# Kernel optimization log

Measured on AMD Instinct MI355X. Metric: run time of the kernel, lower is better.

The kernel has to match this reference:

```python
import jax, jax.numpy as jnp
import numpy as np

N_Q = 32      # questions per batch
N_DOCS = 8    # docs per question (positive first)
Q_LEN = 32    # query tokens
D_LEN = 200   # doc tokens
DIM = 128     # ColBERT embedding dim


def setup_inputs() -> dict:
    key = jax.random.key(0)
    k1, k2 = jax.random.split(key)
    hq = jax.random.normal(k1, (N_Q, Q_LEN, DIM), dtype=jnp.float32)
    hd = jax.random.normal(k2, (N_Q * N_DOCS, D_LEN, DIM), dtype=jnp.float32)
    return {"hq": hq, "hd": hd}


def reference(hq, hd):
    # ColBERT maxsim: [n, m, q, d] token-level scores
    scores = jnp.einsum("nqh,mdh->nmqd", hq, hd)
    # max over doc tokens, mean over query tokens -> [n, m]
    score_matrix = jnp.max(scores, axis=-1).mean(axis=-1)

    n, m = score_matrix.shape
    n_docs = m // n
    # positive doc is the first in each group: targets = [0, n_docs, 2*n_docs, ...]
    targets = jnp.arange(0, m, n_docs)
    logp = jax.nn.log_softmax(score_matrix, axis=-1)
    loss = -jnp.mean(jnp.take_along_axis(logp, targets[:, None], axis=1))
    return score_matrix, loss
```

## Files before the change

kernel.cpp:

```cpp
#include <hip/hip_runtime.h>
#include <hip/hip_bf16.h>
#include <math.h>

typedef short short8 __attribute__((ext_vector_type(8)));
typedef float f32x4 __attribute__((ext_vector_type(4)));

#define NQ 32
#define NDOCS 8
#define QLEN 32
#define DLEN 200
#define DIM 128
#define MD 256
#define ROWB 256

__device__ __forceinline__ short f2bf(float x) {
    union { float f; unsigned u; } v; v.f = x;
    unsigned r = v.u + 0x7FFFu + ((v.u >> 16) & 1u);
    return (short)(r >> 16);
}

__device__ __forceinline__ short8 cvt8(float4 f0, float4 f1) {
    short8 o;
    o[0] = f2bf(f0.x); o[1] = f2bf(f0.y); o[2] = f2bf(f0.z); o[3] = f2bf(f0.w);
    o[4] = f2bf(f1.x); o[5] = f2bf(f1.y); o[6] = f2bf(f1.z); o[7] = f2bf(f1.w);
    return o;
}

__device__ __forceinline__ void writeChunk(char* lds, int c, float4 f0, float4 f1) {
    int row = c >> 4, kc = c & 15;
    int byte = row * ROWB + ((kc * 16) ^ ((row & 7) << 4));
    *reinterpret_cast<short8*>(&lds[byte]) = cvt8(f0, f1);
}

__global__ __launch_bounds__(1024, 4) void colbert_scores(const float* __restrict__ hd,
                                                          const float* __restrict__ hq,
                                                          float* __restrict__ out) {
    __shared__ char lds[208 * ROWB];
    const int m = blockIdx.x;
    const int tid = threadIdx.x;
    const float4* src4 = reinterpret_cast<const float4*>(hd + (size_t)m * (DLEN * DIM));

    for (int c = tid; c < 3200; c += 1024) {
        float4 f0 = src4[c * 2], f1 = src4[c * 2 + 1];
        writeChunk(lds, c, f0, f1);
    }
    if (tid < 128) {
        float4 z = {0.f, 0.f, 0.f, 0.f};
        writeChunk(lds, 3200 + tid, z, z);
    }

    const int wid = tid >> 6, lane = tid & 63;
    const int lg = lane >> 4, lr = lane & 15;
    const int n0 = wid * 2;
    const float4* hq4 = reinterpret_cast<const float4*>(hq);
    short8 a[2][2][4];
    #pragma unroll
    for (int nn = 0; nn < 2; ++nn)
        #pragma unroll
        for (int qt = 0; qt < 2; ++qt)
            #pragma unroll
            for (int s = 0; s < 4; ++s) {
                int e4 = ((n0 + nn) * QLEN + qt * 16 + lr) * (DIM / 4) + s * 8 + lg * 2;
                a[nn][qt][s] = cvt8(hq4[e4], hq4[e4 + 1]);
            }

    __syncthreads();

    int va[4];
    const int pre = ((lg ^ (lr & 7)) << 4);
    #pragma unroll
    for (int s = 0; s < 4; ++s) va[s] = lr * ROWB + (pre ^ (s << 6));

    float qmax00 = -INFINITY, qmax01 = -INFINITY, qmax10 = -INFINITY, qmax11 = -INFINITY;

#define STEP(DT, MASKED)                                                          \
    {                                                                             \
        f32x4 acc00 = {0,0,0,0}, acc01 = {0,0,0,0}, acc10 = {0,0,0,0}, acc11 = {0,0,0,0}; \
        _Pragma("unroll")                                                         \
        for (int s = 0; s < 4; ++s) {                                             \
            short8 b = *reinterpret_cast<const short8*>(&lds[va[s] + (DT) * 4096]); \
            acc00 = __builtin_amdgcn_mfma_f32_16x16x32_bf16(b, a[0][0][s], acc00, 0, 0, 0); \
            acc01 = __builtin_amdgcn_mfma_f32_16x16x32_bf16(b, a[0][1][s], acc01, 0, 0, 0); \
            acc10 = __builtin_amdgcn_mfma_f32_16x16x32_bf16(b, a[1][0][s], acc10, 0, 0, 0); \
            acc11 = __builtin_amdgcn_mfma_f32_16x16x32_bf16(b, a[1][1][s], acc11, 0, 0, 0); \
        }                                                                         \
        if (!(MASKED) || lg < 2) {                                                \
            qmax00 = fmaxf(qmax00, fmaxf(fmaxf(acc00[0], acc00[1]), fmaxf(acc00[2], acc00[3]))); \
            qmax01 = fmaxf(qmax01, fmaxf(fmaxf(acc01[0], acc01[1]), fmaxf(acc01[2], acc01[3]))); \
            qmax10 = fmaxf(qmax10, fmaxf(fmaxf(acc10[0], acc10[1]), fmaxf(acc10[2], acc10[3]))); \
            qmax11 = fmaxf(qmax11, fmaxf(fmaxf(acc11[0], acc11[1]), fmaxf(acc11[2], acc11[3]))); \
        }                                                                         \
    }

    #pragma unroll
    for (int dt = 0; dt < 12; ++dt) STEP(dt, false);
    STEP(12, true);
#undef STEP

    #pragma unroll
    for (int off = 16; off <= 32; off <<= 1) {
        qmax00 = fmaxf(qmax00, __shfl_xor(qmax00, off, 64));
        qmax01 = fmaxf(qmax01, __shfl_xor(qmax01, off, 64));
        qmax10 = fmaxf(qmax10, __shfl_xor(qmax10, off, 64));
        qmax11 = fmaxf(qmax11, __shfl_xor(qmax11, off, 64));
    }
    float s0 = qmax00 + qmax01;
    float s1 = qmax10 + qmax11;
    #pragma unroll
    for (int off = 1; off <= 8; off <<= 1) {
        s0 += __shfl_xor(s0, off, 64);
        s1 += __shfl_xor(s1, off, 64);
    }
    if (lane == 0) {
        out[(size_t)n0 * MD + m] = s0 * (1.0f / 32.0f);
        out[(size_t)(n0 + 1) * MD + m] = s1 * (1.0f / 32.0f);
    }
}

__global__ __launch_bounds__(256) void colbert_loss(const float* __restrict__ scores,
                                                    float* __restrict__ loss_out) {
    __shared__ float terms[NQ];
    const int tid = threadIdx.x;
    const int wid = tid >> 6, lane = tid & 63;
    for (int n = wid; n < NQ; n += 4) {
        const float* row = scores + n * MD;
        float v0 = row[lane], v1 = row[64 + lane], v2 = row[128 + lane], v3 = row[192 + lane];
        float mx = fmaxf(fmaxf(v0, v1), fmaxf(v2, v3));
        #pragma unroll
        for (int off = 1; off < 64; off <<= 1) mx = fmaxf(mx, __shfl_xor(mx, off, 64));
        float s = expf(v0 - mx) + expf(v1 - mx) + expf(v2 - mx) + expf(v3 - mx);
        #pragma unroll
        for (int off = 1; off < 64; off <<= 1) s += __shfl_xor(s, off, 64);
        if (lane == 0) terms[n] = (mx + logf(s)) - row[n * NDOCS];
    }
    __syncthreads();
    if (tid == 0) {
        float acc = 0.f;
        #pragma unroll
        for (int n = 0; n < NQ; ++n) acc += terms[n];
        loss_out[0] = acc * (1.0f / NQ);
    }
}

extern "C" void kernel_launch(void* const* d_in, const int* in_sizes, int n_in,
                              void* d_out, int out_size, void* d_ws, size_t ws_size,
                              hipStream_t stream) {
    const float* hq = (const float*)d_in[0];
    const float* hd = (const float*)d_in[1];
    float* out = (float*)d_out;

    colbert_scores<<<MD, 1024, 0, stream>>>(hd, hq, out);
    colbert_loss<<<1, 256, 0, stream>>>(out, out + NQ * MD);
}
```

Baseline: 45.24 us.

## Pre-convert inputs to bf16 in a separate kernel and drop LDS staging

Adds a conversion kernel that writes hq and hd to a bf16 workspace, with hd padded to 208 rows per doc. The scores kernel then loads bf16 MFMA operands straight from global memory with no LDS staging or swizzle. It also splits each doc across 4 blocks of 256 threads, 1024 blocks in total, to raise parallelism beyond one block per doc. In exchange it adds a kernel launch and extra global traffic for the bf16 round trip. The padded rows are never written, so they hold uninitialized data, but they are masked out of the max.

```diff
diff --git a/kernel.cpp b/kernel.cpp
--- a/kernel.cpp
+++ b/kernel.cpp
@@ -11,7 +11,9 @@
 #define DLEN 200
 #define DIM 128
 #define MD 256
-#define ROWB 256
+#define HD_ROWS 208
+#define HQB_ELEMS (NQ * QLEN * DIM)
+#define HDB_OFF_SHORTS HQB_ELEMS
 
 __device__ __forceinline__ short f2bf(float x) {
     union { float f; unsigned u; } v; v.f = x;
@@ -26,86 +28,97 @@
     return o;
 }
 
-__device__ __forceinline__ void writeChunk(char* lds, int c, float4 f0, float4 f1) {
-    int row = c >> 4, kc = c & 15;
-    int byte = row * ROWB + ((kc * 16) ^ ((row & 7) << 4));
-    *reinterpret_cast<short8*>(&lds[byte]) = cvt8(f0, f1);
+__global__ __launch_bounds__(256) void convert_all(const float* __restrict__ hq,
+                                                   const float* __restrict__ hd,
+                                                   short* __restrict__ hqb,
+                                                   short* __restrict__ hdb) {
+    int b = blockIdx.x;
+    if (b < 64) {
+        int idx = b * 256 + threadIdx.x;
+        const float4* p = reinterpret_cast<const float4*>(hq) + (size_t)idx * 2;
+        reinterpret_cast<short8*>(hqb)[idx] = cvt8(p[0], p[1]);
+    } else {
+        int c = (b - 64) * 256 + threadIdx.x;
+        int m = c / 3200;
+        int rkc = c - m * 3200;
+        const float4* p = reinterpret_cast<const float4*>(hd) + (size_t)c * 2;
+        reinterpret_cast<short8*>(hdb)[(size_t)m * (HD_ROWS * 16) + rkc] = cvt8(p[0], p[1]);
+    }
 }
 
-__global__ __launch_bounds__(1024, 4) void colbert_scores(const float* __restrict__ hd,
-                                                          const float* __restrict__ hq,
-                                                          float* __restrict__ out) {
-    __shared__ char lds[208 * ROWB];
-    const int m = blockIdx.x;
+__global__ __launch_bounds__(256, 4) void colbert_scores(const short* __restrict__ hqb,
+                                                         const short* __restrict__ hdb,
+                                                         float* __restrict__ out) {
+    const int b = blockIdx.x;
+    const int m = b & 255, g = b >> 8;
     const int tid = threadIdx.x;
-    const float4* src4 = reinterpret_cast<const float4*>(hd + (size_t)m * (DLEN * DIM));
-
-    for (int c = tid; c < 3200; c += 1024) {
-        float4 f0 = src4[c * 2], f1 = src4[c * 2 + 1];
-        writeChunk(lds, c, f0, f1);
-    }
-    if (tid < 128) {
-        float4 z = {0.f, 0.f, 0.f, 0.f};
-        writeChunk(lds, 3200 + tid, z, z);
-    }
-
     const int wid = tid >> 6, lane = tid & 63;
     const int lg = lane >> 4, lr = lane & 15;
-    const int n0 = wid * 2;
-    const float4* hq4 = reinterpret_cast<const float4*>(hq);
-    short8 a[2][2][4];
+    const int n0 = g * 8 + wid * 2;
+
+    short8 B[2][2][4];
     #pragma unroll
     for (int nn = 0; nn < 2; ++nn)
         #pragma unroll
         for (int qt = 0; qt < 2; ++qt)
             #pragma unroll
-            for (int s = 0; s < 4; ++s) {
-                int e4 = ((n0 + nn) * QLEN + qt * 16 + lr) * (DIM / 4) + s * 8 + lg * 2;
-                a[nn][qt][s] = cvt8(hq4[e4], hq4[e4 + 1]);
-            }
+            for (int s = 0; s < 4; ++s)
+                B[nn][qt][s] = *reinterpret_cast<const short8*>(
+                    hqb + ((size_t)((n0 + nn) * QLEN + qt * 16 + lr) * DIM + s * 32 + lg * 8));
 
-    __syncthreads();
+    const short* hdm = hdb + (size_t)m * (HD_ROWS * DIM);
+    const short* arow = hdm + (size_t)lr * DIM + lg * 8;
 
-    int va[4];
-    const int pre = ((lg ^ (lr & 7)) << 4);
+    float qmax[2][2];
     #pragma unroll
-    for (int s = 0; s < 4; ++s) va[s] = lr * ROWB + (pre ^ (s << 6));
+    for (int nn = 0; nn < 2; ++nn)
+        #pragma unroll
+        for (int qt = 0; qt < 2; ++qt) qmax[nn][qt] = -INFINITY;
 
-    float qmax00 = -INFINITY, qmax01 = -INFINITY, qmax10 = -INFINITY, qmax11 = -INFINITY;
+    #pragma unroll 1
+    for (int dt = 0; dt < 13; ++dt) {
+        short8 A_[4];
+        #pragma unroll
+        for (int s = 0; s < 4; ++s)
+            A_[s] = *reinterpret_cast<const short8*>(arow + (size_t)dt * (16 * DIM) + s * 32);
 
-#define STEP(DT, MASKED)                                                          \
-    {                                                                             \
-        f32x4 acc00 = {0,0,0,0}, acc01 = {0,0,0,0}, acc10 = {0,0,0,0}, acc11 = {0,0,0,0}; \
-        _Pragma("unroll")                                                         \
-        for (int s = 0; s < 4; ++s) {                                             \
-            short8 b = *reinterpret_cast<const short8*>(&lds[va[s] + (DT) * 4096]); \
-            acc00 = __builtin_amdgcn_mfma_f32_16x16x32_bf16(b, a[0][0][s], acc00, 0, 0, 0); \
-            acc01 = __builtin_amdgcn_mfma_f32_16x16x32_bf16(b, a[0][1][s], acc01, 0, 0, 0); \
-            acc10 = __builtin_amdgcn_mfma_f32_16x16x32_bf16(b, a[1][0][s], acc10, 0, 0, 0); \
-            acc11 = __builtin_amdgcn_mfma_f32_16x16x32_bf16(b, a[1][1][s], acc11, 0, 0, 0); \
-        }                                                                         \
-        if (!(MASKED) || lg < 2) {                                                \
-            qmax00 = fmaxf(qmax00, fmaxf(fmaxf(acc00[0], acc00[1]), fmaxf(acc00[2], acc00[3]))); \
-            qmax01 = fmaxf(qmax01, fmaxf(fmaxf(acc01[0], acc01[1]), fmaxf(acc01[2], acc01[3]))); \
-            qmax10 = fmaxf(qmax10, fmaxf(fmaxf(acc10[0], acc10[1]), fmaxf(acc10[2], acc10[3]))); \
-            qmax11 = fmaxf(qmax11, fmaxf(fmaxf(acc11[0], acc11[1]), fmaxf(acc11[2], acc11[3]))); \
-        }                                                                         \
+        f32x4 acc[2][2];
+        #pragma unroll
+        for (int nn = 0; nn < 2; ++nn)
+            #pragma unroll
+            for (int qt = 0; qt < 2; ++qt) acc[nn][qt] = (f32x4){0.f, 0.f, 0.f, 0.f};
+
+        #pragma unroll
+        for (int s = 0; s < 4; ++s)
+            #pragma unroll
+            for (int nn = 0; nn < 2; ++nn)
+                #pragma unroll
+                for (int qt = 0; qt < 2; ++qt)
+                    acc[nn][qt] = __builtin_amdgcn_mfma_f32_16x16x32_bf16(
+                        A_[s], B[nn][qt][s], acc[nn][qt], 0, 0, 0);
+
+        const bool valid = (dt < 12) | (lg < 2);
+        if (valid) {
+            #pragma unroll
+            for (int nn = 0; nn < 2; ++nn)
+                #pragma unroll
+                for (int qt = 0; qt < 2; ++qt)
+                    qmax[nn][qt] = fmaxf(qmax[nn][qt],
+                        fmaxf(fmaxf(acc[nn][qt][0], acc[nn][qt][1]),
+                              fmaxf(acc[nn][qt][2], acc[nn][qt][3])));
+        }
     }
 
     #pragma unroll
-    for (int dt = 0; dt < 12; ++dt) STEP(dt, false);
-    STEP(12, true);
-#undef STEP
+    for (int off = 16; off <= 32; off <<= 1)
+        #pragma unroll
+        for (int nn = 0; nn < 2; ++nn)
+            #pragma unroll
+            for (int qt = 0; qt < 2; ++qt)
+                qmax[nn][qt] = fmaxf(qmax[nn][qt], __shfl_xor(qmax[nn][qt], off, 64));
 
-    #pragma unroll
-    for (int off = 16; off <= 32; off <<= 1) {
-        qmax00 = fmaxf(qmax00, __shfl_xor(qmax00, off, 64));
-        qmax01 = fmaxf(qmax01, __shfl_xor(qmax01, off, 64));
-        qmax10 = fmaxf(qmax10, __shfl_xor(qmax10, off, 64));
-        qmax11 = fmaxf(qmax11, __shfl_xor(qmax11, off, 64));
-    }
-    float s0 = qmax00 + qmax01;
-    float s1 = qmax10 + qmax11;
+    float s0 = qmax[0][0] + qmax[0][1];
+    float s1 = qmax[1][0] + qmax[1][1];
     #pragma unroll
     for (int off = 1; off <= 8; off <<= 1) {
         s0 += __shfl_xor(s0, off, 64);
@@ -148,7 +161,10 @@
     const float* hq = (const float*)d_in[0];
     const float* hd = (const float*)d_in[1];
     float* out = (float*)d_out;
+    short* hqb = (short*)d_ws;
+    short* hdb = (short*)d_ws + HDB_OFF_SHORTS;
 
-    colbert_scores<<<MD, 1024, 0, stream>>>(hd, hq, out);
+    convert_all<<<3264, 256, 0, stream>>>(hq, hd, hqb, hdb);
+    colbert_scores<<<1024, 256, 0, stream>>>(hqb, hdb, out);
     colbert_loss<<<1, 256, 0, stream>>>(out, out + NQ * MD);
 }
```

Result: slower. 52.08 us (+15.1%).
